# Performance work log

Measured on AMD Instinct MI355X. Metric: run time of the kernel, lower is better.

The kernel has to match this reference:

```python
import jax, jax.numpy as jnp
import numpy as np

B, L, D, H = 2, 2048, 2048, 16
HD = D // H  # head dim = 128
EPS = 1e-6


def rms_norm(x, g):
    norm = jax.lax.rsqrt(jnp.mean(x * x, axis=-1, keepdims=True) + EPS)
    return x * norm * g


def setup_inputs() -> dict:
    key = jax.random.key(0)
    ks = jax.random.split(key, 8)
    s = lambda d: 1.0 / np.sqrt(d)
    return {
        "x": jax.random.normal(ks[0], (B, L, D), dtype=jnp.float32),
        "w_qkv": jax.random.normal(ks[1], (3 * D, D), dtype=jnp.float32) * s(D),
        "w_out": jax.random.normal(ks[2], (D, D), dtype=jnp.float32) * s(D),
        "w_in": jax.random.normal(ks[3], (D, D), dtype=jnp.float32) * s(D),
        "w_hidden": jax.random.normal(ks[4], (D, D), dtype=jnp.float32) * s(D),
        "w_gate": jax.random.normal(ks[5], (D, D), dtype=jnp.float32) * s(D),
        "g_attn_norm": jnp.ones((D,), dtype=jnp.float32),
        "g_ffn_norm": jnp.ones((D,), dtype=jnp.float32),
    }


def reference(x, w_qkv, w_out, w_in, w_hidden, w_gate, g_attn_norm, g_ffn_norm):
    # --- attention branch ---
    xn = rms_norm(x, g_attn_norm)
    qkv = jnp.einsum("bld,ed->ble", xn, w_qkv)  # [B, L, 3D]
    q, k, v = jnp.split(qkv, 3, axis=-1)
    split_heads = lambda t: t.reshape(B, L, H, HD).transpose(0, 2, 1, 3)  # b h l k
    q, k, v = split_heads(q), split_heads(k), split_heads(v)
    scores = jnp.einsum("bhqk,bhsk->bhqs", q, k) / jnp.sqrt(jnp.float32(HD))
    scores = jax.nn.softmax(scores, axis=-1)  # [B, H, L, L]
    attn = jnp.einsum("bhqs,bhsk->bhqk", scores, v)
    attn = attn.transpose(0, 2, 1, 3).reshape(B, L, D)
    attn_out = jnp.einsum("bld,ed->ble", attn, w_out)
    after_attn = x + attn_out
    # --- gated FFN branch (note: gate is computed FROM hidden, per source) ---
    yn = rms_norm(after_attn, g_ffn_norm)
    hidden = jax.nn.relu(jnp.einsum("bld,hd->blh", yn, w_in))
    gate = jnp.einsum("blh,gh->blg", hidden, w_gate)
    ffn = jnp.einsum("blh,dh->bld", hidden * gate, w_hidden)
    out = after_attn + ffn
    return out, scores
```

## Files before the change

kernel.cpp:

```cpp
#include <hip/hip_runtime.h>


typedef __bf16 bf16;
typedef bf16 bf16x4 __attribute__((ext_vector_type(4)));
typedef bf16 bf16x8 __attribute__((ext_vector_type(8)));
typedef float f32x4 __attribute__((ext_vector_type(4)));

#define AS1 __attribute__((address_space(1)))
#define AS3 __attribute__((address_space(3)))

__device__ __forceinline__ void load_lds16(const bf16* g, bf16* l) {
  __builtin_amdgcn_global_load_lds((AS1 void*)g, (AS3 void*)l, 16, 0, 0);
}

__global__ __launch_bounds__(256) void f2b(const float* __restrict__ in,
                                           bf16* __restrict__ out, long n) {
  long i = ((long)blockIdx.x * 256 + threadIdx.x) * 4;
  if (i >= n) return;
  float4 v = *(const float4*)(in + i);
  bf16x4 o = {(bf16)v.x, (bf16)v.y, (bf16)v.z, (bf16)v.w};
  *(bf16x4*)(out + i) = o;
}

__global__ __launch_bounds__(256) void rmsnorm_k(const float* __restrict__ x,
                                                 const float* __restrict__ g,
                                                 bf16* __restrict__ o) {
  const long row = blockIdx.x;
  const float* xr = x + row * 2048;
  const int base = threadIdx.x * 8;
  float4 a = *(const float4*)(xr + base);
  float4 b = *(const float4*)(xr + base + 4);
  float ss = a.x * a.x + a.y * a.y + a.z * a.z + a.w * a.w +
             b.x * b.x + b.y * b.y + b.z * b.z + b.w * b.w;
  for (int off = 32; off; off >>= 1) ss += __shfl_down(ss, off, 64);
  __shared__ float red[4];
  const int lane = threadIdx.x & 63, wv = threadIdx.x >> 6;
  if (lane == 0) red[wv] = ss;
  __syncthreads();
  const float tot = red[0] + red[1] + red[2] + red[3];
  const float nrm = rsqrtf(tot * (1.0f / 2048.0f) + 1e-6f);
  float4 ga = *(const float4*)(g + base);
  float4 gb = *(const float4*)(g + base + 4);
  bf16x8 ov = {(bf16)(a.x * nrm * ga.x), (bf16)(a.y * nrm * ga.y),
               (bf16)(a.z * nrm * ga.z), (bf16)(a.w * nrm * ga.w),
               (bf16)(b.x * nrm * gb.x), (bf16)(b.y * nrm * gb.y),
               (bf16)(b.z * nrm * gb.z), (bf16)(b.w * nrm * gb.w)};
  *(bf16x8*)(o + row * 2048 + base) = ov;
}

__global__ __launch_bounds__(256) void softmax_k(float* __restrict__ s) {
  const long row = blockIdx.x;
  float* p = s + row * 2048;
  const int base = threadIdx.x * 8;
  float4 a = *(const float4*)(p + base);
  float4 b = *(const float4*)(p + base + 4);
  float v[8] = {a.x, a.y, a.z, a.w, b.x, b.y, b.z, b.w};
  float mx = v[0];
#pragma unroll
  for (int j = 1; j < 8; j++) mx = fmaxf(mx, v[j]);
  for (int off = 32; off; off >>= 1) mx = fmaxf(mx, __shfl_down(mx, off, 64));
  __shared__ float red[4];
  const int lane = threadIdx.x & 63, wv = threadIdx.x >> 6;
  if (lane == 0) red[wv] = mx;
  __syncthreads();
  mx = fmaxf(fmaxf(red[0], red[1]), fmaxf(red[2], red[3]));
  __syncthreads();
  float sum = 0.f;
#pragma unroll
  for (int j = 0; j < 8; j++) {
    v[j] = __expf(v[j] - mx);
    sum += v[j];
  }
  for (int off = 32; off; off >>= 1) sum += __shfl_down(sum, off, 64);
  if (lane == 0) red[wv] = sum;
  __syncthreads();
  const float inv = 1.0f / (red[0] + red[1] + red[2] + red[3]);
  float4 oa = {v[0] * inv, v[1] * inv, v[2] * inv, v[3] * inv};
  float4 ob = {v[4] * inv, v[5] * inv, v[6] * inv, v[7] * inv};
  *(float4*)(p + base) = oa;
  *(float4*)(p + base + 4) = ob;
}

__global__ __launch_bounds__(256) void transpose_v(const bf16* __restrict__ qkv,
                                                   bf16* __restrict__ vt) {
  __shared__ bf16 t[32][33];
  const int z = blockIdx.z, zb = z >> 4, zh = z & 15;
  const int s0 = blockIdx.x * 32, d0 = blockIdx.y * 32;
  const int tx = threadIdx.x & 31, ty = threadIdx.x >> 5;
#pragma unroll
  for (int i = 0; i < 32; i += 8)
    t[ty + i][tx] =
        qkv[(long)(zb * 2048 + s0 + ty + i) * 6144 + 4096 + zh * 128 + d0 + tx];
  __syncthreads();
#pragma unroll
  for (int i = 0; i < 32; i += 8)
    vt[(long)z * 262144 + (long)(d0 + ty + i) * 2048 + s0 + tx] = t[tx][ty + i];
}

template <bool AF32>
__global__ __launch_bounds__(256) void gemm_bt(
    const void* __restrict__ Ap, long lda, long sAb, long sAh,
    const bf16* __restrict__ Bt, long ldb, long sBb, long sBh, int K,
    float* __restrict__ Cf, bf16* __restrict__ Cb, long ldc, long sCb, long sCh,
    float scale, const float* __restrict__ addf, const bf16* __restrict__ mulb,
    int relu) {
  __shared__ __align__(16) bf16 ldsA[128 * 32];
  __shared__ __align__(16) bf16 ldsB[128 * 32];

  const int tid = threadIdx.x;
  const int lane = tid & 63;
  const int wv = tid >> 6;
  const int wm = (wv >> 1) << 6;
  const int wn = (wv & 1) << 6;
  const int fr = lane & 15;
  const int ko = (lane >> 4) << 3;

  const long m0 = (long)blockIdx.x * 128;
  const long n0 = (long)blockIdx.y * 128;
  const int zb = blockIdx.z >> 4, zh = blockIdx.z & 15;

  const bf16* Abf = nullptr;
  const float* Af = nullptr;
  if (AF32)
    Af = (const float*)Ap + (long)zb * sAb + (long)zh * sAh;
  else
    Abf = (const bf16*)Ap + (long)zb * sAb + (long)zh * sAh;
  const bf16* B = Bt + (long)zb * sBb + (long)zh * sBh;

  const int c0 = tid, c1 = tid + 256;
  const int r0 = c0 >> 2, kk0 = (c0 & 3) << 3;
  const int r1 = c1 >> 2, kk1 = (c1 & 3) << 3;

  f32x4 acc[4][4] = {};

  for (int k0 = 0; k0 < K; k0 += 32) {
    if (AF32) {
      const float* g0 = Af + (m0 + r0) * lda + k0 + kk0;
      float4 u0 = *(const float4*)g0;
      float4 v0 = *(const float4*)(g0 + 4);
      const float* g1 = Af + (m0 + r1) * lda + k0 + kk1;
      float4 u1 = *(const float4*)g1;
      float4 v1 = *(const float4*)(g1 + 4);
      bf16x8 w0 = {(bf16)u0.x, (bf16)u0.y, (bf16)u0.z, (bf16)u0.w,
                   (bf16)v0.x, (bf16)v0.y, (bf16)v0.z, (bf16)v0.w};
      bf16x8 w1 = {(bf16)u1.x, (bf16)u1.y, (bf16)u1.z, (bf16)u1.w,
                   (bf16)v1.x, (bf16)v1.y, (bf16)v1.z, (bf16)v1.w};
      *(bf16x8*)&ldsA[c0 * 8] = w0;
      *(bf16x8*)&ldsA[c1 * 8] = w1;
    } else {
      load_lds16(Abf + (m0 + r0) * lda + k0 + kk0, &ldsA[c0 * 8]);
      load_lds16(Abf + (m0 + r1) * lda + k0 + kk1, &ldsA[c1 * 8]);
    }
    load_lds16(B + (n0 + r0) * ldb + k0 + kk0, &ldsB[c0 * 8]);
    load_lds16(B + (n0 + r1) * ldb + k0 + kk1, &ldsB[c1 * 8]);
    __syncthreads();

    bf16x8 af[4], bfr[4];
#pragma unroll
    for (int i = 0; i < 4; ++i)
      af[i] = *(const bf16x8*)&ldsA[(wm + i * 16 + fr) * 32 + ko];
#pragma unroll
    for (int j = 0; j < 4; ++j)
      bfr[j] = *(const bf16x8*)&ldsB[(wn + j * 16 + fr) * 32 + ko];
#pragma unroll
    for (int i = 0; i < 4; ++i)
#pragma unroll
      for (int j = 0; j < 4; ++j)
        acc[i][j] =
            __builtin_amdgcn_mfma_f32_16x16x32_bf16(af[i], bfr[j], acc[i][j], 0, 0, 0);
    __syncthreads();
  }

  const long coff = (long)zb * sCb + (long)zh * sCh;
#pragma unroll
  for (int i = 0; i < 4; ++i) {
#pragma unroll
    for (int r = 0; r < 4; ++r) {
      const long row = m0 + wm + i * 16 + ((lane >> 4) << 2) + r;
#pragma unroll
      for (int j = 0; j < 4; ++j) {
        const long col = n0 + wn + j * 16 + (lane & 15);
        const long idx = coff + row * ldc + col;
        float v = acc[i][j][r] * scale;
        if (addf) v += addf[idx];
        if (mulb) v *= (float)mulb[idx];
        if (relu) v = fmaxf(v, 0.f);
        if (Cf)
          Cf[idx] = v;
        else
          Cb[idx] = (bf16)v;
      }
    }
  }
}

extern "C" void kernel_launch(void* const* d_in, const int* in_sizes, int n_in,
                              void* d_out, int out_size, void* d_ws,
                              size_t ws_size, hipStream_t stream) {
  (void)in_sizes; (void)n_in; (void)out_size; (void)ws_size;
  const float* x      = (const float*)d_in[0];
  const float* w_qkv  = (const float*)d_in[1];
  const float* w_out  = (const float*)d_in[2];
  const float* w_in   = (const float*)d_in[3];
  const float* w_hid  = (const float*)d_in[4];
  const float* w_gate = (const float*)d_in[5];
  const float* g_attn = (const float*)d_in[6];
  const float* g_ffn  = (const float*)d_in[7];

  float* outp   = (float*)d_out;
  float* scores = outp + 8388608;

  char* ws = (char*)d_ws;
  bf16* wbuf   = (bf16*)(ws);
  bf16* xn     = (bf16*)(ws + 25165824);
  bf16* qkvb   = (bf16*)(ws + 41943040);
  bf16* attnb  = (bf16*)(ws + 92274688);
  float* after = (float*)(ws + 109051904);
  bf16* vt     = xn;
  bf16* yn     = xn;
  bf16* hidden = qkvb;
  bf16* hg     = (bf16*)(ws + 58720256);

  dim3 blk(256);

  f2b<<<12288, blk, 0, stream>>>(w_qkv, wbuf, 12582912L);
  rmsnorm_k<<<4096, blk, 0, stream>>>(x, g_attn, xn);

  gemm_bt<false><<<dim3(32, 48, 1), blk, 0, stream>>>(
      (const void*)xn, 2048L, 0L, 0L, wbuf, 2048L, 0L, 0L, 2048,
      (float*)nullptr, qkvb, 6144L, 0L, 0L, 1.0f, nullptr, nullptr, 0);

  transpose_v<<<dim3(64, 4, 32), blk, 0, stream>>>(qkvb, vt);

  gemm_bt<false><<<dim3(16, 16, 32), blk, 0, stream>>>(
      (const void*)qkvb, 6144L, 12582912L, 128L,
      qkvb + 2048, 6144L, 12582912L, 128L, 128,
      scores, (bf16*)nullptr, 2048L, 67108864L, 4194304L,
      0.08838834764831845f, nullptr, nullptr, 0);

  softmax_k<<<65536, blk, 0, stream>>>(scores);

  gemm_bt<true><<<dim3(16, 1, 32), blk, 0, stream>>>(
      (const void*)scores, 2048L, 67108864L, 4194304L,
      vt, 2048L, 4194304L, 262144L, 2048,
      (float*)nullptr, attnb, 2048L, 4194304L, 128L, 1.0f, nullptr, nullptr, 0);

  f2b<<<4096, blk, 0, stream>>>(w_out, wbuf, 4194304L);
  gemm_bt<false><<<dim3(32, 16, 1), blk, 0, stream>>>(
      (const void*)attnb, 2048L, 0L, 0L, wbuf, 2048L, 0L, 0L, 2048,
      after, (bf16*)nullptr, 2048L, 0L, 0L, 1.0f, x, nullptr, 0);

  rmsnorm_k<<<4096, blk, 0, stream>>>(after, g_ffn, yn);

  f2b<<<4096, blk, 0, stream>>>(w_in, wbuf, 4194304L);
  gemm_bt<false><<<dim3(32, 16, 1), blk, 0, stream>>>(
      (const void*)yn, 2048L, 0L, 0L, wbuf, 2048L, 0L, 0L, 2048,
      (float*)nullptr, hidden, 2048L, 0L, 0L, 1.0f, nullptr, nullptr, 1);

  f2b<<<4096, blk, 0, stream>>>(w_gate, wbuf, 4194304L);
  gemm_bt<false><<<dim3(32, 16, 1), blk, 0, stream>>>(
      (const void*)hidden, 2048L, 0L, 0L, wbuf, 2048L, 0L, 0L, 2048,
      (float*)nullptr, hg, 2048L, 0L, 0L, 1.0f, nullptr, hidden, 0);

  f2b<<<4096, blk, 0, stream>>>(w_hid, wbuf, 4194304L);
  gemm_bt<false><<<dim3(32, 16, 1), blk, 0, stream>>>(
      (const void*)hg, 2048L, 0L, 0L, wbuf, 2048L, 0L, 0L, 2048,
      outp, (bf16*)nullptr, 2048L, 0L, 0L, 1.0f, after, nullptr, 0);
}
```

Measured before the change: 1.519 ms.

## Fuse softmax into QK^T epilogue and PV prologue via atomic row sums

Removes the standalone softmax kernel. The QK^T GEMM epilogue now writes exp(score) without max subtraction and atomically accumulates per-row sums. The PV GEMM normalizes each row by its sum while loading A, then writes the normalized scores back in place. This saves one full read-write pass over the 512MB scores tensor. The cost is dropping max subtraction, which risks overflow for large logits, plus extra atomics and a zero-init kernel.

```diff
diff --git a/kernel.cpp b/kernel.cpp
--- a/kernel.cpp
+++ b/kernel.cpp
@@ -11,6 +11,10 @@
 
 __device__ __forceinline__ void load_lds16(const bf16* g, bf16* l) {
   __builtin_amdgcn_global_load_lds((AS1 void*)g, (AS3 void*)l, 16, 0, 0);
+}
+
+__global__ __launch_bounds__(256) void zero_k(float* __restrict__ p) {
+  p[blockIdx.x * 256 + threadIdx.x] = 0.f;
 }
 
 __global__ __launch_bounds__(256) void f2b(const float* __restrict__ in,
@@ -48,39 +52,6 @@
   *(bf16x8*)(o + row * 2048 + base) = ov;
 }
 
-__global__ __launch_bounds__(256) void softmax_k(float* __restrict__ s) {
-  const long row = blockIdx.x;
-  float* p = s + row * 2048;
-  const int base = threadIdx.x * 8;
-  float4 a = *(const float4*)(p + base);
-  float4 b = *(const float4*)(p + base + 4);
-  float v[8] = {a.x, a.y, a.z, a.w, b.x, b.y, b.z, b.w};
-  float mx = v[0];
-#pragma unroll
-  for (int j = 1; j < 8; j++) mx = fmaxf(mx, v[j]);
-  for (int off = 32; off; off >>= 1) mx = fmaxf(mx, __shfl_down(mx, off, 64));
-  __shared__ float red[4];
-  const int lane = threadIdx.x & 63, wv = threadIdx.x >> 6;
-  if (lane == 0) red[wv] = mx;
-  __syncthreads();
-  mx = fmaxf(fmaxf(red[0], red[1]), fmaxf(red[2], red[3]));
-  __syncthreads();
-  float sum = 0.f;
-#pragma unroll
-  for (int j = 0; j < 8; j++) {
-    v[j] = __expf(v[j] - mx);
-    sum += v[j];
-  }
-  for (int off = 32; off; off >>= 1) sum += __shfl_down(sum, off, 64);
-  if (lane == 0) red[wv] = sum;
-  __syncthreads();
-  const float inv = 1.0f / (red[0] + red[1] + red[2] + red[3]);
-  float4 oa = {v[0] * inv, v[1] * inv, v[2] * inv, v[3] * inv};
-  float4 ob = {v[4] * inv, v[5] * inv, v[6] * inv, v[7] * inv};
-  *(float4*)(p + base) = oa;
-  *(float4*)(p + base + 4) = ob;
-}
-
 __global__ __launch_bounds__(256) void transpose_v(const bf16* __restrict__ qkv,
                                                    bf16* __restrict__ vt) {
   __shared__ bf16 t[32][33];
@@ -97,13 +68,13 @@
     vt[(long)z * 262144 + (long)(d0 + ty + i) * 2048 + s0 + tx] = t[tx][ty + i];
 }
 
-template <bool AF32>
+template <int AMODE, int EXPM>
 __global__ __launch_bounds__(256) void gemm_bt(
     const void* __restrict__ Ap, long lda, long sAb, long sAh,
     const bf16* __restrict__ Bt, long ldb, long sBb, long sBh, int K,
     float* __restrict__ Cf, bf16* __restrict__ Cb, long ldc, long sCb, long sCh,
     float scale, const float* __restrict__ addf, const bf16* __restrict__ mulb,
-    int relu) {
+    int relu, float* rowsum, float* Awr) {
   __shared__ __align__(16) bf16 ldsA[128 * 32];
   __shared__ __align__(16) bf16 ldsB[128 * 32];
 
@@ -121,26 +92,41 @@
 
   const bf16* Abf = nullptr;
   const float* Af = nullptr;
-  if (AF32)
+  float* Aw = nullptr;
+  if constexpr (AMODE == 0) {
+    Abf = (const bf16*)Ap + (long)zb * sAb + (long)zh * sAh;
+  } else {
     Af = (const float*)Ap + (long)zb * sAb + (long)zh * sAh;
-  else
-    Abf = (const bf16*)Ap + (long)zb * sAb + (long)zh * sAh;
+    Aw = Awr + (long)zb * sAb + (long)zh * sAh;
+  }
   const bf16* B = Bt + (long)zb * sBb + (long)zh * sBh;
 
   const int c0 = tid, c1 = tid + 256;
   const int r0 = c0 >> 2, kk0 = (c0 & 3) << 3;
   const int r1 = c1 >> 2, kk1 = (c1 & 3) << 3;
 
+  float inv0 = 0.f, inv1 = 0.f;
+  if constexpr (AMODE == 2) {
+    const long rb = (long)blockIdx.z * 2048;
+    inv0 = 1.0f / rowsum[rb + m0 + r0];
+    inv1 = 1.0f / rowsum[rb + m0 + r1];
+  }
+
   f32x4 acc[4][4] = {};
 
   for (int k0 = 0; k0 < K; k0 += 32) {
-    if (AF32) {
+    float4 u0, v0, u1, v1;
+    if constexpr (AMODE == 2) {
       const float* g0 = Af + (m0 + r0) * lda + k0 + kk0;
-      float4 u0 = *(const float4*)g0;
-      float4 v0 = *(const float4*)(g0 + 4);
+      u0 = *(const float4*)g0;
+      v0 = *(const float4*)(g0 + 4);
       const float* g1 = Af + (m0 + r1) * lda + k0 + kk1;
-      float4 u1 = *(const float4*)g1;
-      float4 v1 = *(const float4*)(g1 + 4);
+      u1 = *(const float4*)g1;
+      v1 = *(const float4*)(g1 + 4);
+      u0.x *= inv0; u0.y *= inv0; u0.z *= inv0; u0.w *= inv0;
+      v0.x *= inv0; v0.y *= inv0; v0.z *= inv0; v0.w *= inv0;
+      u1.x *= inv1; u1.y *= inv1; u1.z *= inv1; u1.w *= inv1;
+      v1.x *= inv1; v1.y *= inv1; v1.z *= inv1; v1.w *= inv1;
       bf16x8 w0 = {(bf16)u0.x, (bf16)u0.y, (bf16)u0.z, (bf16)u0.w,
                    (bf16)v0.x, (bf16)v0.y, (bf16)v0.z, (bf16)v0.w};
       bf16x8 w1 = {(bf16)u1.x, (bf16)u1.y, (bf16)u1.z, (bf16)u1.w,
@@ -155,6 +141,15 @@
     load_lds16(B + (n0 + r1) * ldb + k0 + kk1, &ldsB[c1 * 8]);
     __syncthreads();
 
+    if constexpr (AMODE == 2) {
+      float* s0 = Aw + (m0 + r0) * lda + k0 + kk0;
+      *(float4*)s0 = u0;
+      *(float4*)(s0 + 4) = v0;
+      float* s1 = Aw + (m0 + r1) * lda + k0 + kk1;
+      *(float4*)s1 = u1;
+      *(float4*)(s1 + 4) = v1;
+    }
+
     bf16x8 af[4], bfr[4];
 #pragma unroll
     for (int i = 0; i < 4; ++i)
@@ -172,23 +167,47 @@
   }
 
   const long coff = (long)zb * sCb + (long)zh * sCh;
-#pragma unroll
-  for (int i = 0; i < 4; ++i) {
-#pragma unroll
-    for (int r = 0; r < 4; ++r) {
-      const long row = m0 + wm + i * 16 + ((lane >> 4) << 2) + r;
-#pragma unroll
-      for (int j = 0; j < 4; ++j) {
-        const long col = n0 + wn + j * 16 + (lane & 15);
-        const long idx = coff + row * ldc + col;
-        float v = acc[i][j][r] * scale;
-        if (addf) v += addf[idx];
-        if (mulb) v *= (float)mulb[idx];
-        if (relu) v = fmaxf(v, 0.f);
-        if (Cf)
-          Cf[idx] = v;
-        else
-          Cb[idx] = (bf16)v;
+  if constexpr (EXPM) {
+    const long rb = (long)blockIdx.z * 2048;
+#pragma unroll
+    for (int i = 0; i < 4; ++i) {
+#pragma unroll
+      for (int r = 0; r < 4; ++r) {
+        const long row = m0 + wm + i * 16 + ((lane >> 4) << 2) + r;
+        float es = 0.f;
+#pragma unroll
+        for (int j = 0; j < 4; ++j) {
+          const long col = n0 + wn + j * 16 + (lane & 15);
+          const float e = __expf(acc[i][j][r] * scale);
+          Cf[coff + row * ldc + col] = e;
+          es += e;
+        }
+        es += __shfl_xor(es, 1, 64);
+        es += __shfl_xor(es, 2, 64);
+        es += __shfl_xor(es, 4, 64);
+        es += __shfl_xor(es, 8, 64);
+        if ((lane & 15) == 0) atomicAdd(rowsum + rb + row, es);
+      }
+    }
+  } else {
+#pragma unroll
+    for (int i = 0; i < 4; ++i) {
+#pragma unroll
+      for (int r = 0; r < 4; ++r) {
+        const long row = m0 + wm + i * 16 + ((lane >> 4) << 2) + r;
+#pragma unroll
+        for (int j = 0; j < 4; ++j) {
+          const long col = n0 + wn + j * 16 + (lane & 15);
+          const long idx = coff + row * ldc + col;
+          float v = acc[i][j][r] * scale;
+          if (addf) v += addf[idx];
+          if (mulb) v *= (float)mulb[idx];
+          if (relu) v = fmaxf(v, 0.f);
+          if (Cf)
+            Cf[idx] = v;
+          else
+            Cb[idx] = (bf16)v;
+        }
       }
     }
   }
@@ -220,50 +239,57 @@
   bf16* yn     = xn;
   bf16* hidden = qkvb;
   bf16* hg     = (bf16*)(ws + 58720256);
+  float* rowsum = after;
 
   dim3 blk(256);
+
+  zero_k<<<256, blk, 0, stream>>>(rowsum);
 
   f2b<<<12288, blk, 0, stream>>>(w_qkv, wbuf, 12582912L);
   rmsnorm_k<<<4096, blk, 0, stream>>>(x, g_attn, xn);
 
-  gemm_bt<false><<<dim3(32, 48, 1), blk, 0, stream>>>(
+  gemm_bt<0, 0><<<dim3(32, 48, 1), blk, 0, stream>>>(
       (const void*)xn, 2048L, 0L, 0L, wbuf, 2048L, 0L, 0L, 2048,
-      (float*)nullptr, qkvb, 6144L, 0L, 0L, 1.0f, nullptr, nullptr, 0);
+      (float*)nullptr, qkvb, 6144L, 0L, 0L, 1.0f, nullptr, nullptr, 0,
+      nullptr, nullptr);
 
   transpose_v<<<dim3(64, 4, 32), blk, 0, stream>>>(qkvb, vt);
 
-  gemm_bt<false><<<dim3(16, 16, 32), blk, 0, stream>>>(
+  gemm_bt<0, 1><<<dim3(16, 16, 32), blk, 0, stream>>>(
       (const void*)qkvb, 6144L, 12582912L, 128L,
       qkvb + 2048, 6144L, 12582912L, 128L, 128,
       scores, (bf16*)nullptr, 2048L, 67108864L, 4194304L,
-      0.08838834764831845f, nullptr, nullptr, 0);
-
-  softmax_k<<<65536, blk, 0, stream>>>(scores);
-
-  gemm_bt<true><<<dim3(16, 1, 32), blk, 0, stream>>>(
+      0.08838834764831845f, nullptr, nullptr, 0, rowsum, nullptr);
+
+  gemm_bt<2, 0><<<dim3(16, 1, 32), blk, 0, stream>>>(
       (const void*)scores, 2048L, 67108864L, 4194304L,
       vt, 2048L, 4194304L, 262144L, 2048,
-      (float*)nullptr, attnb, 2048L, 4194304L, 128L, 1.0f, nullptr, nullptr, 0);
+      (float*)nullptr, attnb, 2048L, 4194304L, 128L, 1.0f, nullptr, nullptr, 0,
+      rowsum, scores);
 
   f2b<<<4096, blk, 0, stream>>>(w_out, wbuf, 4194304L);
-  gemm_bt<false><<<dim3(32, 16, 1), blk, 0, stream>>>(
+  gemm_bt<0, 0><<<dim3(32, 16, 1), blk, 0, stream>>>(
       (const void*)attnb, 2048L, 0L, 0L, wbuf, 2048L, 0L, 0L, 2048,
-      after, (bf16*)nullptr, 2048L, 0L, 0L, 1.0f, x, nullptr, 0);
+      after, (bf16*)nullptr, 2048L, 0L, 0L, 1.0f, x, nullptr, 0,
+      nullptr, nullptr);
 
   rmsnorm_k<<<4096, blk, 0, stream>>>(after, g_ffn, yn);
 
   f2b<<<4096, blk, 0, stream>>>(w_in, wbuf, 4194304L);
-  gemm_bt<false><<<dim3(32, 16, 1), blk, 0, stream>>>(
+  gemm_bt<0, 0><<<dim3(32, 16, 1), blk, 0, stream>>>(
       (const void*)yn, 2048L, 0L, 0L, wbuf, 2048L, 0L, 0L, 2048,
-      (float*)nullptr, hidden, 2048L, 0L, 0L, 1.0f, nullptr, nullptr, 1);
+      (float*)nullptr, hidden, 2048L, 0L, 0L, 1.0f, nullptr, nullptr, 1,
+      nullptr, nullptr);
 
   f2b<<<4096, blk, 0, stream>>>(w_gate, wbuf, 4194304L);
-  gemm_bt<false><<<dim3(32, 16, 1), blk, 0, stream>>>(
+  gemm_bt<0, 0><<<dim3(32, 16, 1), blk, 0, stream>>>(
       (const void*)hidden, 2048L, 0L, 0L, wbuf, 2048L, 0L, 0L, 2048,
-      (float*)nullptr, hg, 2048L, 0L, 0L, 1.0f, nullptr, hidden, 0);
+      (float*)nullptr, hg, 2048L, 0L, 0L, 1.0f, nullptr, hidden, 0,
+      nullptr, nullptr);
 
   f2b<<<4096, blk, 0, stream>>>(w_hid, wbuf, 4194304L);
-  gemm_bt<false><<<dim3(32, 16, 1), blk, 0, stream>>>(
+  gemm_bt<0, 0><<<dim3(32, 16, 1), blk, 0, stream>>>(
       (const void*)hg, 2048L, 0L, 0L, wbuf, 2048L, 0L, 0L, 2048,
-      outp, (bf16*)nullptr, 2048L, 0L, 0L, 1.0f, after, nullptr, 0);
-}
+      outp, (bf16*)nullptr, 2048L, 0L, 0L, 1.0f, after, nullptr, 0,
+      nullptr, nullptr);
+}
```

After: 1.440 ms. 5.2% less time.
